# Kernel optimization log

Measured on AMD Instinct MI355X. Metric: run time of the kernel, lower is better.

## Reference

```python
import jax, jax.numpy as jnp
import numpy as np

B, S, D = 2, 1024, 768
H, HD = 12, 64
E, K, F = 8, 2, 3072
EPS = 1e-5


def _ln(x, g, b):
    mu = jnp.mean(x, -1, keepdims=True)
    var = jnp.mean(jnp.square(x - mu), -1, keepdims=True)
    return (x - mu) * jax.lax.rsqrt(var + EPS) * g + b


def setup_inputs() -> dict:
    key = jax.random.key(0)
    ks = jax.random.split(key, 12)
    s = lambda k, shape, sc: jax.random.normal(k, shape, jnp.float32) * sc
    return {
        "hidden_states": s(ks[0], (B, S, D), 1.0),
        "ln1_g": jnp.ones((D,), jnp.float32), "ln1_b": jnp.zeros((D,), jnp.float32),
        "w_attn": s(ks[1], (D, 3 * D), 0.02), "b_attn": jnp.zeros((3 * D,), jnp.float32),
        "w_attnproj": s(ks[2], (D, D), 0.02), "b_attnproj": jnp.zeros((D,), jnp.float32),
        "ln2_g": jnp.ones((D,), jnp.float32), "ln2_b": jnp.zeros((D,), jnp.float32),
        "w_router": s(ks[3], (E, D), 0.01),
        "w_fc": s(ks[4], (E, D, F), 0.02 / E), "b_fc": jnp.zeros((E, F), jnp.float32),
        "w_proj": s(ks[5], (E, F, D), 0.02 / E), "b_proj": jnp.zeros((E, D), jnp.float32),
    }


def reference(hidden_states, ln1_g, ln1_b, w_attn, b_attn, w_attnproj, b_attnproj,
              ln2_g, ln2_b, w_router, w_fc, b_fc, w_proj, b_proj):
    # --- attention sub-block (GPT-2 style, causal) ---
    residual = hidden_states
    x = _ln(hidden_states, ln1_g, ln1_b)
    qkv = x @ w_attn + b_attn                         # [B,S,3D]
    q, k, v = jnp.split(qkv, 3, axis=-1)
    def heads(t):
        return t.reshape(B, S, H, HD).transpose(0, 2, 1, 3)  # [B,H,S,HD]
    q, k, v = heads(q), heads(k), heads(v)
    scores = jnp.einsum("bhqd,bhkd->bhqk", q, k) / np.sqrt(HD).astype(np.float32)
    causal = jnp.tril(jnp.ones((S, S), bool))
    scores = jnp.where(causal, scores, jnp.finfo(scores.dtype).min)
    attn = jax.nn.softmax(scores, axis=-1)
    ctx = jnp.einsum("bhqk,bhkd->bhqd", attn, v)
    ctx = ctx.transpose(0, 2, 1, 3).reshape(B, S, D)
    attn_out = ctx @ w_attnproj + b_attnproj
    hs = attn_out + residual

    # --- MoE FFN sub-block ---
    residual = hs
    x2 = _ln(hs, ln2_g, ln2_b)
    logits = x2 @ w_router.T                          # [B,S,E]
    probs = jax.nn.softmax(logits, axis=-1)
    top_w, top_idx = jax.lax.top_k(probs, K)          # [B,S,K]
    top_w = top_w / jnp.sum(top_w, -1, keepdims=True)
    gates = jnp.sum(jax.nn.one_hot(top_idx, E, dtype=x2.dtype) * top_w[..., None], axis=2)  # [B,S,E]
    h = jax.nn.gelu(jnp.einsum("bsd,edf->bsef", x2, w_fc) + b_fc, approximate=False)
    y = jnp.einsum("bsef,efd->bsed", h, w_proj) + b_proj
    moe_out = jnp.einsum("bse,bsed->bsd", gates, y)
    return moe_out + residual
```

## Files before the change

### kernel.cpp

```cpp
#include <hip/hip_runtime.h>
#include <hip/hip_bf16.h>
#include <math.h>

#define NB 2
#define SEQ 1024
#define DM 768
#define NHEAD 12
#define HDIM 64
#define NEXP 8
#define FF 3072
#define NTOK (NB*SEQ)
#define TDIM (3*DM)
#define LNEPS 1e-5f

typedef __attribute__((ext_vector_type(8))) short v8s;
typedef __attribute__((ext_vector_type(4))) float v4f;

#define GLDS16(src, dst) \
    __builtin_amdgcn_global_load_lds((const __attribute__((address_space(1))) unsigned int*)(src), \
                                     (__attribute__((address_space(3))) unsigned int*)(dst), 16, 0, 0)

static __device__ __forceinline__ float bf2f(unsigned short u){
    return __uint_as_float(((unsigned)u) << 16);
}
static __device__ __forceinline__ unsigned short f2bf(float f){
    unsigned u = __float_as_uint(f);
    u += 0x7fffu + ((u >> 16) & 1u);
    return (unsigned short)(u >> 16);
}
static __device__ __forceinline__ float gelu_exact(float x){
    return 0.5f * x * (1.0f + erff(x * 0.70710678118654752440f));
}

__global__ __launch_bounds__(256) void tconv_kernel(const float* __restrict__ in,
                                                    unsigned short* __restrict__ out,
                                                    int R, int C){
    __shared__ float T[32][33];
    size_t base = (size_t)blockIdx.z * R * C;
    int c0 = blockIdx.x * 32, r0 = blockIdx.y * 32;
    int t = threadIdx.x;
    int tr = t >> 3, tc4 = (t & 7) * 4;
    float4 v = *(const float4*)&in[base + (size_t)(r0 + tr) * C + c0 + tc4];
    T[tr][tc4+0] = v.x; T[tr][tc4+1] = v.y; T[tr][tc4+2] = v.z; T[tr][tc4+3] = v.w;
    __syncthreads();
    int oc = t >> 3, or4 = (t & 7) * 4;
    ushort4 o;
    o.x = f2bf(T[or4+0][oc]); o.y = f2bf(T[or4+1][oc]);
    o.z = f2bf(T[or4+2][oc]); o.w = f2bf(T[or4+3][oc]);
    *(ushort4*)&out[base + (size_t)(c0 + oc) * R + r0 + or4] = o;
}

__global__ __launch_bounds__(256) void ln_kernel(const float* __restrict__ in,
                                                 const float* __restrict__ g,
                                                 const float* __restrict__ b,
                                                 float* __restrict__ out,
                                                 unsigned short* __restrict__ outb){
    int t = blockIdx.x;
    const float* row = in + (size_t)t * DM;
    int tid = threadIdx.x;
    float v0 = row[tid], v1 = row[tid + 256], v2 = row[tid + 512];
    float s  = v0 + v1 + v2;
    float ss = v0*v0 + v1*v1 + v2*v2;
    for (int off = 32; off; off >>= 1){
        s  += __shfl_down(s, off);
        ss += __shfl_down(ss, off);
    }
    __shared__ float ls[4], lss[4];
    int wid = tid >> 6, lane = tid & 63;
    if (lane == 0){ ls[wid] = s; lss[wid] = ss; }
    __syncthreads();
    if (tid == 0){
        float a = ls[0] + ls[1] + ls[2] + ls[3];
        float c = lss[0] + lss[1] + lss[2] + lss[3];
        float mu = a / (float)DM;
        float var = c / (float)DM - mu * mu;
        ls[0] = mu; lss[0] = rsqrtf(var + LNEPS);
    }
    __syncthreads();
    float mu = ls[0], rs = lss[0];
    float* orow = out + (size_t)t * DM;
    unsigned short* obrow = outb + (size_t)t * DM;
    float o0 = (v0 - mu) * rs * g[tid]       + b[tid];
    float o1 = (v1 - mu) * rs * g[tid + 256] + b[tid + 256];
    float o2 = (v2 - mu) * rs * g[tid + 512] + b[tid + 512];
    orow[tid] = o0; orow[tid+256] = o1; orow[tid+512] = o2;
    obrow[tid] = f2bf(o0); obrow[tid+256] = f2bf(o1); obrow[tid+512] = f2bf(o2);
}


__global__ __launch_bounds__(256) void mm_qkv(const unsigned short* __restrict__ Ab,
                                              const unsigned short* __restrict__ Bb,
                                              const float* __restrict__ bias,
                                              float* __restrict__ C){
    __shared__ __align__(16) unsigned short As[128*32];
    __shared__ __align__(16) unsigned short Bs[128*32];
    int bm = blockIdx.y * 128, bn = blockIdx.x * 128;
    int tid = threadIdx.x, wave = tid >> 6, lane = tid & 63;
    int quad = lane >> 4, l15 = lane & 15;
    int wm = wave >> 1, wn = wave & 1;
    int lrow = lane >> 2, lchunk = (lane & 3) * 8;
    const unsigned short* aS0 = Ab + (size_t)(bm +      wave*16 + lrow) * 768 + lchunk;
    const unsigned short* aS1 = Ab + (size_t)(bm + 64 + wave*16 + lrow) * 768 + lchunk;
    const unsigned short* bS0 = Bb + (size_t)(bn +      wave*16 + lrow) * 768 + lchunk;
    const unsigned short* bS1 = Bb + (size_t)(bn + 64 + wave*16 + lrow) * 768 + lchunk;
    unsigned short* aD0 = &As[(     wave*16)*32];
    unsigned short* aD1 = &As[(64 + wave*16)*32];
    unsigned short* bD0 = &Bs[(     wave*16)*32];
    unsigned short* bD1 = &Bs[(64 + wave*16)*32];
    v4f acc[4][4];
    #pragma unroll
    for (int i = 0; i < 4; i++)
        #pragma unroll
        for (int j = 0; j < 4; j++) acc[i][j] = (v4f){0.f,0.f,0.f,0.f};
    for (int kt = 0; kt < 768/32; kt++){
        int kb = kt * 32;
        GLDS16(aS0 + kb, aD0); GLDS16(aS1 + kb, aD1);
        GLDS16(bS0 + kb, bD0); GLDS16(bS1 + kb, bD1);
        __syncthreads();
        v8s a[4], b[4];
        #pragma unroll
        for (int i = 0; i < 4; i++){
            a[i] = *(const v8s*)&As[(wm*64 + i*16 + l15)*32 + quad*8];
            b[i] = *(const v8s*)&Bs[(wn*64 + i*16 + l15)*32 + quad*8];
        }
        #pragma unroll
        for (int mt = 0; mt < 4; mt++)
            #pragma unroll
            for (int nt = 0; nt < 4; nt++)
                acc[mt][nt] = __builtin_amdgcn_mfma_f32_16x16x32_bf16(a[mt], b[nt], acc[mt][nt], 0, 0, 0);
        __syncthreads();
    }
    #pragma unroll
    for (int nt = 0; nt < 4; nt++){
        int n = bn + wn*64 + nt*16 + l15;
        float bb = bias[n];
        #pragma unroll
        for (int mt = 0; mt < 4; mt++){
            int m = bm + wm*64 + mt*16 + quad*4;
            #pragma unroll
            for (int r = 0; r < 4; r++)
                C[(size_t)(m + r) * TDIM + n] = acc[mt][nt][r] + bb;
        }
    }
}

__global__ __launch_bounds__(256) void mm_attnproj(const unsigned short* __restrict__ Ab,
                                                   const unsigned short* __restrict__ Bb,
                                                   const float* __restrict__ bias,
                                                   const float* __restrict__ res,
                                                   float* __restrict__ C){
    __shared__ __align__(16) unsigned short As[128*32];
    __shared__ __align__(16) unsigned short Bs[128*32];
    int bm = blockIdx.y * 128, bn = blockIdx.x * 128;
    int tid = threadIdx.x, wave = tid >> 6, lane = tid & 63;
    int quad = lane >> 4, l15 = lane & 15;
    int wm = wave >> 1, wn = wave & 1;
    int lrow = lane >> 2, lchunk = (lane & 3) * 8;
    const unsigned short* aS0 = Ab + (size_t)(bm +      wave*16 + lrow) * 768 + lchunk;
    const unsigned short* aS1 = Ab + (size_t)(bm + 64 + wave*16 + lrow) * 768 + lchunk;
    const unsigned short* bS0 = Bb + (size_t)(bn +      wave*16 + lrow) * 768 + lchunk;
    const unsigned short* bS1 = Bb + (size_t)(bn + 64 + wave*16 + lrow) * 768 + lchunk;
    unsigned short* aD0 = &As[(     wave*16)*32];
    unsigned short* aD1 = &As[(64 + wave*16)*32];
    unsigned short* bD0 = &Bs[(     wave*16)*32];
    unsigned short* bD1 = &Bs[(64 + wave*16)*32];
    v4f acc[4][4];
    #pragma unroll
    for (int i = 0; i < 4; i++)
        #pragma unroll
        for (int j = 0; j < 4; j++) acc[i][j] = (v4f){0.f,0.f,0.f,0.f};
    for (int kt = 0; kt < 768/32; kt++){
        int kb = kt * 32;
        GLDS16(aS0 + kb, aD0); GLDS16(aS1 + kb, aD1);
        GLDS16(bS0 + kb, bD0); GLDS16(bS1 + kb, bD1);
        __syncthreads();
        v8s a[4], b[4];
        #pragma unroll
        for (int i = 0; i < 4; i++){
            a[i] = *(const v8s*)&As[(wm*64 + i*16 + l15)*32 + quad*8];
            b[i] = *(const v8s*)&Bs[(wn*64 + i*16 + l15)*32 + quad*8];
        }
        #pragma unroll
        for (int mt = 0; mt < 4; mt++)
            #pragma unroll
            for (int nt = 0; nt < 4; nt++)
                acc[mt][nt] = __builtin_amdgcn_mfma_f32_16x16x32_bf16(a[mt], b[nt], acc[mt][nt], 0, 0, 0);
        __syncthreads();
    }
    #pragma unroll
    for (int nt = 0; nt < 4; nt++){
        int n = bn + wn*64 + nt*16 + l15;
        float bb = bias[n];
        #pragma unroll
        for (int mt = 0; mt < 4; mt++){
            int m = bm + wm*64 + mt*16 + quad*4;
            #pragma unroll
            for (int r = 0; r < 4; r++)
                C[(size_t)(m + r) * DM + n] = acc[mt][nt][r] + bb + res[(size_t)(m + r) * DM + n];
        }
    }
}

__global__ __launch_bounds__(256) void mm_fc(const unsigned short* __restrict__ Xb,
                                             const unsigned short* __restrict__ Wb,
                                             const float* __restrict__ bfc,
                                             const int* __restrict__ expTok,
                                             const int* __restrict__ cnt,
                                             const int* __restrict__ offE,
                                             unsigned short* __restrict__ H){
    int e = blockIdx.z, tile = blockIdx.y;
    int c = cnt[e];
    int rows = c - tile * 128;
    if (rows <= 0) return;
    __shared__ __align__(16) unsigned short As[128*32];
    __shared__ __align__(16) unsigned short Bs[128*32];
    __shared__ int toks[128];
    int bn = blockIdx.x * 128;
    int tid = threadIdx.x, wave = tid >> 6, lane = tid & 63;
    if (tid < 128){
        int idx = tile * 128 + tid;
        if (idx >= c) idx = c - 1;
        toks[tid] = expTok[e * NTOK + idx];
    }
    __syncthreads();
    int quad = lane >> 4, l15 = lane & 15;
    int wm = wave >> 1, wn = wave & 1;
    int lrow = lane >> 2, lchunk = (lane & 3) * 8;
    int tok0 = toks[     wave*16 + lrow];
    int tok1 = toks[64 + wave*16 + lrow];
    const unsigned short* Be = Wb + (size_t)e * FF * DM;
    const unsigned short* aS0 = Xb + (size_t)tok0 * 768 + lchunk;
    const unsigned short* aS1 = Xb + (size_t)tok1 * 768 + lchunk;
    const unsigned short* bS0 = Be + (size_t)(bn +      wave*16 + lrow) * 768 + lchunk;
    const unsigned short* bS1 = Be + (size_t)(bn + 64 + wave*16 + lrow) * 768 + lchunk;
    unsigned short* aD0 = &As[(     wave*16)*32];
    unsigned short* aD1 = &As[(64 + wave*16)*32];
    unsigned short* bD0 = &Bs[(     wave*16)*32];
    unsigned short* bD1 = &Bs[(64 + wave*16)*32];
    v4f acc[4][4];
    #pragma unroll
    for (int i = 0; i < 4; i++)
        #pragma unroll
        for (int j = 0; j < 4; j++) acc[i][j] = (v4f){0.f,0.f,0.f,0.f};
    for (int kt = 0; kt < 768/32; kt++){
        int kb = kt * 32;
        GLDS16(aS0 + kb, aD0); GLDS16(aS1 + kb, aD1);
        GLDS16(bS0 + kb, bD0); GLDS16(bS1 + kb, bD1);
        __syncthreads();
        v8s a[4], b[4];
        #pragma unroll
        for (int i = 0; i < 4; i++){
            a[i] = *(const v8s*)&As[(wm*64 + i*16 + l15)*32 + quad*8];
            b[i] = *(const v8s*)&Bs[(wn*64 + i*16 + l15)*32 + quad*8];
        }
        #pragma unroll
        for (int mt = 0; mt < 4; mt++)
            #pragma unroll
            for (int nt = 0; nt < 4; nt++)
                acc[mt][nt] = __builtin_amdgcn_mfma_f32_16x16x32_bf16(a[mt], b[nt], acc[mt][nt], 0, 0, 0);
        __syncthreads();
    }
    int slot0 = offE[e] + tile * 128;
    #pragma unroll
    for (int nt = 0; nt < 4; nt++){
        int n = bn + wn*64 + nt*16 + l15;
        float bb = bfc[(size_t)e * FF + n];
        #pragma unroll
        for (int mt = 0; mt < 4; mt++){
            int ml = wm*64 + mt*16 + quad*4;
            #pragma unroll
            for (int r = 0; r < 4; r++)
                if (ml + r < rows)
                    H[(size_t)(slot0 + ml + r) * FF + n] = f2bf(gelu_exact(acc[mt][nt][r] + bb));
        }
    }
}

__global__ __launch_bounds__(256) void mm_proj(const unsigned short* __restrict__ H,
                                               const unsigned short* __restrict__ Wb,
                                               const int* __restrict__ cnt,
                                               const int* __restrict__ offE,
                                               float* __restrict__ Y){
    int e = blockIdx.z, tile = blockIdx.y;
    int c = cnt[e];
    int rows = c - tile * 128;
    if (rows <= 0) return;
    __shared__ __align__(16) unsigned short As[128*32];
    __shared__ __align__(16) unsigned short Bs[128*32];
    int bn = blockIdx.x * 128;
    int tid = threadIdx.x, wave = tid >> 6, lane = tid & 63;
    int quad = lane >> 4, l15 = lane & 15;
    int wm = wave >> 1, wn = wave & 1;
    int lrow = lane >> 2, lchunk = (lane & 3) * 8;
    int slot0 = offE[e] + tile * 128;
    int rl0 =      wave*16 + lrow; if (rl0 > rows - 1) rl0 = rows - 1;
    int rl1 = 64 + wave*16 + lrow; if (rl1 > rows - 1) rl1 = rows - 1;
    const unsigned short* Be = Wb + (size_t)e * DM * FF;
    const unsigned short* aS0 = H + (size_t)(slot0 + rl0) * FF + lchunk;
    const unsigned short* aS1 = H + (size_t)(slot0 + rl1) * FF + lchunk;
    const unsigned short* bS0 = Be + (size_t)(bn +      wave*16 + lrow) * FF + lchunk;
    const unsigned short* bS1 = Be + (size_t)(bn + 64 + wave*16 + lrow) * FF + lchunk;
    unsigned short* aD0 = &As[(     wave*16)*32];
    unsigned short* aD1 = &As[(64 + wave*16)*32];
    unsigned short* bD0 = &Bs[(     wave*16)*32];
    unsigned short* bD1 = &Bs[(64 + wave*16)*32];
    v4f acc[4][4];
    #pragma unroll
    for (int i = 0; i < 4; i++)
        #pragma unroll
        for (int j = 0; j < 4; j++) acc[i][j] = (v4f){0.f,0.f,0.f,0.f};
    for (int kt = 0; kt < FF/32; kt++){
        int kb = kt * 32;
        GLDS16(aS0 + kb, aD0); GLDS16(aS1 + kb, aD1);
        GLDS16(bS0 + kb, bD0); GLDS16(bS1 + kb, bD1);
        __syncthreads();
        v8s a[4], b[4];
        #pragma unroll
        for (int i = 0; i < 4; i++){
            a[i] = *(const v8s*)&As[(wm*64 + i*16 + l15)*32 + quad*8];
            b[i] = *(const v8s*)&Bs[(wn*64 + i*16 + l15)*32 + quad*8];
        }
        #pragma unroll
        for (int mt = 0; mt < 4; mt++)
            #pragma unroll
            for (int nt = 0; nt < 4; nt++)
                acc[mt][nt] = __builtin_amdgcn_mfma_f32_16x16x32_bf16(a[mt], b[nt], acc[mt][nt], 0, 0, 0);
        __syncthreads();
    }
    #pragma unroll
    for (int nt = 0; nt < 4; nt++){
        int n = bn + wn*64 + nt*16 + l15;
        #pragma unroll
        for (int mt = 0; mt < 4; mt++){
            int ml = wm*64 + mt*16 + quad*4;
            #pragma unroll
            for (int r = 0; r < 4; r++)
                if (ml + r < rows)
                    Y[(size_t)(slot0 + ml + r) * DM + n] = acc[mt][nt][r];
        }
    }
}

__global__ __launch_bounds__(256) void attn_prep(const float* __restrict__ qkv,
                                                 unsigned short* __restrict__ Qb,
                                                 unsigned short* __restrict__ Kb,
                                                 unsigned short* __restrict__ Vt){
    int bi = blockIdx.x;
    int c = bi & 15, bh = bi >> 4;
    int h = bh % NHEAD, b = bh / NHEAD;
    __shared__ float vt[64][65];
    int tid = threadIdx.x;
    int row = tid >> 2, ds = (tid & 3) * 16;
    const float* base = qkv + (size_t)(b*SEQ + c*64 + row) * TDIM + h*HDIM + ds;
    size_t qkrow = ((size_t)bh*SEQ + c*64 + row) * HDIM + ds;
    #pragma unroll
    for (int j = 0; j < 16; j += 4){
        float4 qv = *(const float4*)(base + j);
        ushort4 qo;
        qo.x = f2bf(qv.x*0.125f); qo.y = f2bf(qv.y*0.125f);
        qo.z = f2bf(qv.z*0.125f); qo.w = f2bf(qv.w*0.125f);
        *(ushort4*)&Qb[qkrow + j] = qo;
        float4 kv = *(const float4*)(base + DM + j);
        ushort4 ko;
        ko.x = f2bf(kv.x); ko.y = f2bf(kv.y); ko.z = f2bf(kv.z); ko.w = f2bf(kv.w);
        *(ushort4*)&Kb[qkrow + j] = ko;
        float4 vv = *(const float4*)(base + 2*DM + j);
        vt[row][ds+j+0] = vv.x; vt[row][ds+j+1] = vv.y;
        vt[row][ds+j+2] = vv.z; vt[row][ds+j+3] = vv.w;
    }
    __syncthreads();
    int d = tid >> 2, ks = (tid & 3) * 16;
    size_t vrow = ((size_t)bh*HDIM + d) * SEQ + c*64 + ks;
    #pragma unroll
    for (int j = 0; j < 16; j += 4){
        ushort4 o;
        o.x = f2bf(vt[ks+j+0][d]); o.y = f2bf(vt[ks+j+1][d]);
        o.z = f2bf(vt[ks+j+2][d]); o.w = f2bf(vt[ks+j+3][d]);
        *(ushort4*)&Vt[vrow + j] = o;
    }
}

__global__ __launch_bounds__(64) void fattn(const unsigned short* __restrict__ Qb,
                                            const unsigned short* __restrict__ Kb,
                                            const unsigned short* __restrict__ Vt,
                                            unsigned short* __restrict__ ctxb){
    int bh = blockIdx.x >> 6;
    int q0 = (63 - (blockIdx.x & 63)) * 16;
    int h = bh % NHEAD, b = bh / NHEAD;
    int lane = threadIdx.x;
    int quad = lane >> 4, l15 = lane & 15;

    __shared__ __align__(16) unsigned short Plds[16*32];

    const unsigned short* qp = Qb + ((size_t)bh*SEQ + q0 + l15) * HDIM + quad*8;
    v8s qa0 = *(const v8s*)qp;
    v8s qa1 = *(const v8s*)(qp + 32);

    v4f o0 = {0,0,0,0}, o1 = {0,0,0,0}, o2 = {0,0,0,0}, o3 = {0,0,0,0};
    float mrow[4] = {-1e30f,-1e30f,-1e30f,-1e30f};
    float lrow[4] = {0,0,0,0};

    int nch = (q0 + 16 + 31) >> 5;
    for (int ch = 0; ch < nch; ch++){
        int kt = ch * 32;
        const unsigned short* kp = Kb + ((size_t)bh*SEQ + kt + l15) * HDIM + quad*8;
        v8s kb0l = *(const v8s*)kp;
        v8s kb0h = *(const v8s*)(kp + 32);
        v8s kb1l = *(const v8s*)(kp + 16*HDIM);
        v8s kb1h = *(const v8s*)(kp + 16*HDIM + 32);
        v4f s0 = {0,0,0,0}, s1 = {0,0,0,0};
        s0 = __builtin_amdgcn_mfma_f32_16x16x32_bf16(qa0, kb0l, s0, 0, 0, 0);
        s0 = __builtin_amdgcn_mfma_f32_16x16x32_bf16(qa1, kb0h, s0, 0, 0, 0);
        s1 = __builtin_amdgcn_mfma_f32_16x16x32_bf16(qa0, kb1l, s1, 0, 0, 0);
        s1 = __builtin_amdgcn_mfma_f32_16x16x32_bf16(qa1, kb1h, s1, 0, 0, 0);

        int key0 = kt + l15, key1 = kt + 16 + l15;
        float alpha[4];
        #pragma unroll
        for (int r = 0; r < 4; r++){
            int qrow = q0 + quad*4 + r;
            float v0 = (key0 <= qrow) ? s0[r] : -1e30f;
            float v1 = (key1 <= qrow) ? s1[r] : -1e30f;
            float mx = fmaxf(v0, v1);
            mx = fmaxf(mx, __shfl_xor(mx, 1));
            mx = fmaxf(mx, __shfl_xor(mx, 2));
            mx = fmaxf(mx, __shfl_xor(mx, 4));
            mx = fmaxf(mx, __shfl_xor(mx, 8));
            float mn = fmaxf(mrow[r], mx);
            alpha[r] = __expf(mrow[r] - mn);
            float p0 = __expf(v0 - mn);
            float p1 = __expf(v1 - mn);
            float ps = p0 + p1;
            ps += __shfl_xor(ps, 1);
            ps += __shfl_xor(ps, 2);
            ps += __shfl_xor(ps, 4);
            ps += __shfl_xor(ps, 8);
            lrow[r] = lrow[r] * alpha[r] + ps;
            mrow[r] = mn;
            Plds[(quad*4 + r)*32 + l15]      = f2bf(p0);
            Plds[(quad*4 + r)*32 + 16 + l15] = f2bf(p1);
        }
        #pragma unroll
        for (int r = 0; r < 4; r++){
            o0[r] *= alpha[r]; o1[r] *= alpha[r];
            o2[r] *= alpha[r]; o3[r] *= alpha[r];
        }
        __syncthreads();
        v8s pa = *(const v8s*)&Plds[l15*32 + quad*8];
        const unsigned short* vp = Vt + ((size_t)bh*HDIM + l15) * SEQ + kt + quad*8;
        v8s vb0 = *(const v8s*)vp;
        v8s vb1 = *(const v8s*)(vp + 16*SEQ);
        v8s vb2 = *(const v8s*)(vp + 32*SEQ);
        v8s vb3 = *(const v8s*)(vp + 48*SEQ);
        o0 = __builtin_amdgcn_mfma_f32_16x16x32_bf16(pa, vb0, o0, 0, 0, 0);
        o1 = __builtin_amdgcn_mfma_f32_16x16x32_bf16(pa, vb1, o1, 0, 0, 0);
        o2 = __builtin_amdgcn_mfma_f32_16x16x32_bf16(pa, vb2, o2, 0, 0, 0);
        o3 = __builtin_amdgcn_mfma_f32_16x16x32_bf16(pa, vb3, o3, 0, 0, 0);
        __syncthreads();
    }
    #pragma unroll
    for (int r = 0; r < 4; r++){
        float inv = 1.0f / lrow[r];
        size_t orow = (size_t)(b*SEQ + q0 + quad*4 + r) * DM + h*HDIM;
        ctxb[orow + l15]      = f2bf(o0[r] * inv);
        ctxb[orow + 16 + l15] = f2bf(o1[r] * inv);
        ctxb[orow + 32 + l15] = f2bf(o2[r] * inv);
        ctxb[orow + 48 + l15] = f2bf(o3[r] * inv);
    }
}

__global__ __launch_bounds__(64) void router_kernel(const float* __restrict__ x2,
                                                    const float* __restrict__ wr,
                                                    int* __restrict__ cnt,
                                                    int* __restrict__ expTok,
                                                    int* __restrict__ tokE,
                                                    int* __restrict__ tokPos,
                                                    float* __restrict__ tokGate){
    int t = blockIdx.x;
    int lane = threadIdx.x;
    const float* xr = x2 + (size_t)t * DM;
    float acc[NEXP] = {};
    for (int d = lane; d < DM; d += 64){
        float xv = xr[d];
        #pragma unroll
        for (int e = 0; e < NEXP; e++) acc[e] += xv * wr[e*DM + d];
    }
    #pragma unroll
    for (int e = 0; e < NEXP; e++)
        for (int off = 32; off; off >>= 1) acc[e] += __shfl_xor(acc[e], off);
    if (lane == 0){
        int i0 = 0; float m0 = acc[0];
        #pragma unroll
        for (int e = 1; e < NEXP; e++) if (acc[e] > m0){ m0 = acc[e]; i0 = e; }
        int i1 = -1; float m1 = -INFINITY;
        #pragma unroll
        for (int e = 0; e < NEXP; e++) if (e != i0 && acc[e] > m1){ m1 = acc[e]; i1 = e; }
        float mx = fmaxf(m0, m1);
        float e0 = __expf(m0 - mx), e1 = __expf(m1 - mx);
        float inv = 1.0f / (e0 + e1);
        int p0 = atomicAdd(&cnt[i0], 1);
        int p1 = atomicAdd(&cnt[i1], 1);
        expTok[i0*NTOK + p0] = t;
        expTok[i1*NTOK + p1] = t;
        tokE[t*2]   = i0; tokE[t*2+1]   = i1;
        tokPos[t*2] = p0; tokPos[t*2+1] = p1;
        tokGate[t*2]   = e0 * inv;
        tokGate[t*2+1] = e1 * inv;
    }
}

__global__ void offsets_kernel(const int* __restrict__ cnt, int* __restrict__ offE){
    if (threadIdx.x == 0 && blockIdx.x == 0){
        int a = 0;
        for (int e = 0; e < NEXP; e++){ offE[e] = a; a += cnt[e]; }
    }
}

__global__ __launch_bounds__(256) void combine_kernel(const float* __restrict__ hs,
                                                      const float* __restrict__ Y,
                                                      const float* __restrict__ bproj,
                                                      const int* __restrict__ tokE,
                                                      const int* __restrict__ tokPos,
                                                      const float* __restrict__ tokGate,
                                                      const int* __restrict__ offE,
                                                      float* __restrict__ out){
    int t = blockIdx.x;
    int e0 = tokE[t*2], e1 = tokE[t*2+1];
    int s0 = offE[e0] + tokPos[t*2];
    int s1 = offE[e1] + tokPos[t*2+1];
    float g0 = tokGate[t*2], g1 = tokGate[t*2+1];
    const float* y0 = Y + (size_t)s0 * DM;
    const float* y1 = Y + (size_t)s1 * DM;
    const float* b0 = bproj + (size_t)e0 * DM;
    const float* b1 = bproj + (size_t)e1 * DM;
    const float* hr = hs + (size_t)t * DM;
    float* orow = out + (size_t)t * DM;
    for (int d = threadIdx.x; d < DM; d += 256){
        orow[d] = hr[d] + g0 * (y0[d] + b0[d]) + g1 * (y1[d] + b1[d]);
    }
}

extern "C" void kernel_launch(void* const* d_in, const int* in_sizes, int n_in,
                              void* d_out, int out_size, void* d_ws, size_t ws_size,
                              hipStream_t stream){
    (void)in_sizes; (void)n_in; (void)out_size; (void)ws_size;
    const float* hidden  = (const float*)d_in[0];
    const float* ln1_g   = (const float*)d_in[1];
    const float* ln1_b   = (const float*)d_in[2];
    const float* w_attn  = (const float*)d_in[3];
    const float* b_attn  = (const float*)d_in[4];
    const float* w_aproj = (const float*)d_in[5];
    const float* b_aproj = (const float*)d_in[6];
    const float* ln2_g   = (const float*)d_in[7];
    const float* ln2_b   = (const float*)d_in[8];
    const float* w_rout  = (const float*)d_in[9];
    const float* w_fc    = (const float*)d_in[10];
    const float* b_fc    = (const float*)d_in[11];
    const float* w_proj  = (const float*)d_in[12];
    const float* b_proj  = (const float*)d_in[13];
    float* out = (float*)d_out;

    char* ws = (char*)d_ws;
    float*          x    = (float*)(ws + 0);
    unsigned short* Vt   = (unsigned short*)(ws + 6291456);
    unsigned short* ctxb = (unsigned short*)(ws + 9437184);
    float*          Y    = (float*)(ws + 0);
    float*          hs   = (float*)(ws + 12582912);
    unsigned short* xb   = (unsigned short*)(ws + 18874368);
    float*          qkv  = (float*)(ws + 22020096);
    unsigned short* Qb   = (unsigned short*)(ws + 40894464);
    unsigned short* Kb   = (unsigned short*)(ws + 44040192);
    unsigned short* H    = (unsigned short*)(ws + 22020096);
    unsigned short* Wab  = (unsigned short*)(ws + 47185920);
    unsigned short* Wapb = (unsigned short*)(ws + 50724864);
    unsigned short* Wfcb = (unsigned short*)(ws + 51904512);
    unsigned short* Wprb = (unsigned short*)(ws + 89653248);
    char* rt = ws + 127401984;
    int* cnt      = (int*)(rt + 0);
    int* offE     = (int*)(rt + 64);
    int* expTok   = (int*)(rt + 128);
    int* tokE     = (int*)(rt + 128 + 65536);
    int* tokPos   = (int*)(rt + 128 + 81920);
    float* tokGate= (float*)(rt + 128 + 98304);

    hipMemsetAsync(cnt, 0, NEXP * sizeof(int), stream);

    tconv_kernel<<<dim3(TDIM/32, DM/32, 1), 256, 0, stream>>>(w_attn, Wab, DM, TDIM);
    tconv_kernel<<<dim3(DM/32, DM/32, 1), 256, 0, stream>>>(w_aproj, Wapb, DM, DM);
    tconv_kernel<<<dim3(FF/32, DM/32, NEXP), 256, 0, stream>>>(w_fc, Wfcb, DM, FF);
    tconv_kernel<<<dim3(DM/32, FF/32, NEXP), 256, 0, stream>>>(w_proj, Wprb, FF, DM);

    ln_kernel<<<NTOK, 256, 0, stream>>>(hidden, ln1_g, ln1_b, x, xb);
    mm_qkv<<<dim3(TDIM/128, NTOK/128), 256, 0, stream>>>(xb, Wab, b_attn, qkv);
    attn_prep<<<NB*NHEAD*16, 256, 0, stream>>>(qkv, Qb, Kb, Vt);
    fattn<<<NB*NHEAD*64, 64, 0, stream>>>(Qb, Kb, Vt, ctxb);
    mm_attnproj<<<dim3(DM/128, NTOK/128), 256, 0, stream>>>(ctxb, Wapb, b_aproj, hidden, hs);
    ln_kernel<<<NTOK, 256, 0, stream>>>(hs, ln2_g, ln2_b, x, xb);
    router_kernel<<<NTOK, 64, 0, stream>>>(x, w_rout, cnt, expTok, tokE, tokPos, tokGate);
    offsets_kernel<<<1, 64, 0, stream>>>(cnt, offE);
    mm_fc<<<dim3(FF/128, NTOK/128, NEXP), 256, 0, stream>>>(xb, Wfcb, b_fc, expTok, cnt, offE, H);
    mm_proj<<<dim3(DM/128, NTOK/128, NEXP), 256, 0, stream>>>(H, Wprb, cnt, offE, Y);
    combine_kernel<<<NTOK, 256, 0, stream>>>(hs, Y, b_proj, tokE, tokPos, tokGate, offE, out);
}
```

Baseline: 520.2 us.

## Fuse QKV epilogue into head layout, fuse LN with router, retile GEMMs, split-K proj

The QKV GEMM now writes bf16 Q (prescaled), K and transposed V directly, which removes the fp32 qkv buffer and the attn_prep kernel. The second layernorm is fused with the router, so the fp32 normalized activations are no longer written out. Flash attention now processes 32 query rows per wave and attnproj/qkv use smaller tiles for more blocks. The expert down-projection is split along K into two partial outputs that the combine kernel sums. Together these cut launches and intermediate memory traffic, at the cost of extra partial-sum reads and more complex indexing.

```diff
diff --git a/kernel.cpp b/kernel.cpp
--- a/kernel.cpp
+++ b/kernel.cpp
@@ -12,6 +12,7 @@
 #define NTOK (NB*SEQ)
 #define TDIM (3*DM)
 #define LNEPS 1e-5f
+#define NSLOT (NTOK*2)
 
 typedef __attribute__((ext_vector_type(8))) short v8s;
 typedef __attribute__((ext_vector_type(4))) float v4f;
@@ -50,11 +51,10 @@
     *(ushort4*)&out[base + (size_t)(c0 + oc) * R + r0 + or4] = o;
 }
 
-__global__ __launch_bounds__(256) void ln_kernel(const float* __restrict__ in,
-                                                 const float* __restrict__ g,
-                                                 const float* __restrict__ b,
-                                                 float* __restrict__ out,
-                                                 unsigned short* __restrict__ outb){
+__global__ __launch_bounds__(256) void ln_b(const float* __restrict__ in,
+                                            const float* __restrict__ g,
+                                            const float* __restrict__ b,
+                                            unsigned short* __restrict__ outb){
     int t = blockIdx.x;
     const float* row = in + (size_t)t * DM;
     int tid = threadIdx.x;
@@ -78,68 +78,264 @@
     }
     __syncthreads();
     float mu = ls[0], rs = lss[0];
-    float* orow = out + (size_t)t * DM;
     unsigned short* obrow = outb + (size_t)t * DM;
+    obrow[tid]     = f2bf((v0 - mu) * rs * g[tid]       + b[tid]);
+    obrow[tid+256] = f2bf((v1 - mu) * rs * g[tid + 256] + b[tid + 256]);
+    obrow[tid+512] = f2bf((v2 - mu) * rs * g[tid + 512] + b[tid + 512]);
+}
+
+__global__ __launch_bounds__(256) void ln_router(const float* __restrict__ in,
+                                                 const float* __restrict__ g,
+                                                 const float* __restrict__ b,
+                                                 const float* __restrict__ wr,
+                                                 unsigned short* __restrict__ outb,
+                                                 int* __restrict__ cnt,
+                                                 int* __restrict__ expTok,
+                                                 int* __restrict__ tokE,
+                                                 int* __restrict__ tokPos,
+                                                 float* __restrict__ tokGate){
+    int t = blockIdx.x;
+    const float* row = in + (size_t)t * DM;
+    int tid = threadIdx.x;
+    float v0 = row[tid], v1 = row[tid + 256], v2 = row[tid + 512];
+    float s  = v0 + v1 + v2;
+    float ss = v0*v0 + v1*v1 + v2*v2;
+    for (int off = 32; off; off >>= 1){
+        s  += __shfl_down(s, off);
+        ss += __shfl_down(ss, off);
+    }
+    __shared__ float ls[4], lss[4];
+    __shared__ float wsum[4][NEXP];
+    int wid = tid >> 6, lane = tid & 63;
+    if (lane == 0){ ls[wid] = s; lss[wid] = ss; }
+    __syncthreads();
+    if (tid == 0){
+        float a = ls[0] + ls[1] + ls[2] + ls[3];
+        float c = lss[0] + lss[1] + lss[2] + lss[3];
+        float mu = a / (float)DM;
+        float var = c / (float)DM - mu * mu;
+        ls[0] = mu; lss[0] = rsqrtf(var + LNEPS);
+    }
+    __syncthreads();
+    float mu = ls[0], rs = lss[0];
     float o0 = (v0 - mu) * rs * g[tid]       + b[tid];
     float o1 = (v1 - mu) * rs * g[tid + 256] + b[tid + 256];
     float o2 = (v2 - mu) * rs * g[tid + 512] + b[tid + 512];
-    orow[tid] = o0; orow[tid+256] = o1; orow[tid+512] = o2;
+    unsigned short* obrow = outb + (size_t)t * DM;
     obrow[tid] = f2bf(o0); obrow[tid+256] = f2bf(o1); obrow[tid+512] = f2bf(o2);
-}
-
+    float p[NEXP];
+    #pragma unroll
+    for (int e = 0; e < NEXP; e++)
+        p[e] = o0*wr[e*DM + tid] + o1*wr[e*DM + tid + 256] + o2*wr[e*DM + tid + 512];
+    #pragma unroll
+    for (int e = 0; e < NEXP; e++)
+        for (int off = 32; off; off >>= 1) p[e] += __shfl_down(p[e], off);
+    if (lane == 0){
+        #pragma unroll
+        for (int e = 0; e < NEXP; e++) wsum[wid][e] = p[e];
+    }
+    __syncthreads();
+    if (tid == 0){
+        float lg[NEXP];
+        #pragma unroll
+        for (int e = 0; e < NEXP; e++)
+            lg[e] = wsum[0][e] + wsum[1][e] + wsum[2][e] + wsum[3][e];
+        int i0 = 0; float m0 = lg[0];
+        #pragma unroll
+        for (int e = 1; e < NEXP; e++) if (lg[e] > m0){ m0 = lg[e]; i0 = e; }
+        int i1 = -1; float m1 = -INFINITY;
+        #pragma unroll
+        for (int e = 0; e < NEXP; e++) if (e != i0 && lg[e] > m1){ m1 = lg[e]; i1 = e; }
+        float mx = fmaxf(m0, m1);
+        float e0 = __expf(m0 - mx), e1 = __expf(m1 - mx);
+        float inv = 1.0f / (e0 + e1);
+        int p0 = atomicAdd(&cnt[i0], 1);
+        int p1 = atomicAdd(&cnt[i1], 1);
+        expTok[i0*NTOK + p0] = t;
+        expTok[i1*NTOK + p1] = t;
+        tokE[t*2]   = i0; tokE[t*2+1]   = i1;
+        tokPos[t*2] = p0; tokPos[t*2+1] = p1;
+        tokGate[t*2]   = e0 * inv;
+        tokGate[t*2+1] = e1 * inv;
+    }
+}
 
 __global__ __launch_bounds__(256) void mm_qkv(const unsigned short* __restrict__ Ab,
                                               const unsigned short* __restrict__ Bb,
                                               const float* __restrict__ bias,
-                                              float* __restrict__ C){
-    __shared__ __align__(16) unsigned short As[128*32];
+                                              unsigned short* __restrict__ Qb,
+                                              unsigned short* __restrict__ Kb,
+                                              unsigned short* __restrict__ Vt){
+    __shared__ __align__(16) unsigned short As[64*32];
     __shared__ __align__(16) unsigned short Bs[128*32];
-    int bm = blockIdx.y * 128, bn = blockIdx.x * 128;
+    int bm = blockIdx.y * 64, bn = blockIdx.x * 128;
     int tid = threadIdx.x, wave = tid >> 6, lane = tid & 63;
     int quad = lane >> 4, l15 = lane & 15;
     int wm = wave >> 1, wn = wave & 1;
+    int arow = tid >> 2, achunk = (tid & 3) * 8;
     int lrow = lane >> 2, lchunk = (lane & 3) * 8;
-    const unsigned short* aS0 = Ab + (size_t)(bm +      wave*16 + lrow) * 768 + lchunk;
-    const unsigned short* aS1 = Ab + (size_t)(bm + 64 + wave*16 + lrow) * 768 + lchunk;
-    const unsigned short* bS0 = Bb + (size_t)(bn +      wave*16 + lrow) * 768 + lchunk;
-    const unsigned short* bS1 = Bb + (size_t)(bn + 64 + wave*16 + lrow) * 768 + lchunk;
-    unsigned short* aD0 = &As[(     wave*16)*32];
-    unsigned short* aD1 = &As[(64 + wave*16)*32];
+    const unsigned short* aS  = Ab + (size_t)(bm + arow) * DM + achunk;
+    const unsigned short* bS0 = Bb + (size_t)(bn +      wave*16 + lrow) * DM + lchunk;
+    const unsigned short* bS1 = Bb + (size_t)(bn + 64 + wave*16 + lrow) * DM + lchunk;
+    unsigned short* aD  = &As[(wave*16)*32];
     unsigned short* bD0 = &Bs[(     wave*16)*32];
     unsigned short* bD1 = &Bs[(64 + wave*16)*32];
-    v4f acc[4][4];
-    #pragma unroll
-    for (int i = 0; i < 4; i++)
+    v4f acc[2][4];
+    #pragma unroll
+    for (int i = 0; i < 2; i++)
         #pragma unroll
         for (int j = 0; j < 4; j++) acc[i][j] = (v4f){0.f,0.f,0.f,0.f};
-    for (int kt = 0; kt < 768/32; kt++){
+    for (int kt = 0; kt < DM/32; kt++){
         int kb = kt * 32;
-        GLDS16(aS0 + kb, aD0); GLDS16(aS1 + kb, aD1);
-        GLDS16(bS0 + kb, bD0); GLDS16(bS1 + kb, bD1);
-        __syncthreads();
-        v8s a[4], b[4];
-        #pragma unroll
-        for (int i = 0; i < 4; i++){
-            a[i] = *(const v8s*)&As[(wm*64 + i*16 + l15)*32 + quad*8];
-            b[i] = *(const v8s*)&Bs[(wn*64 + i*16 + l15)*32 + quad*8];
-        }
-        #pragma unroll
-        for (int mt = 0; mt < 4; mt++)
-            #pragma unroll
-            for (int nt = 0; nt < 4; nt++)
-                acc[mt][nt] = __builtin_amdgcn_mfma_f32_16x16x32_bf16(a[mt], b[nt], acc[mt][nt], 0, 0, 0);
-        __syncthreads();
-    }
-    #pragma unroll
-    for (int nt = 0; nt < 4; nt++){
-        int n = bn + wn*64 + nt*16 + l15;
+        GLDS16(aS + kb, aD); GLDS16(bS0 + kb, bD0); GLDS16(bS1 + kb, bD1);
+        __syncthreads();
+        v8s a[2], bfr[4];
+        #pragma unroll
+        for (int i = 0; i < 2; i++) a[i] = *(const v8s*)&As[(wm*32 + i*16 + l15)*32 + quad*8];
+        #pragma unroll
+        for (int i = 0; i < 4; i++) bfr[i] = *(const v8s*)&Bs[(wn*64 + i*16 + l15)*32 + quad*8];
+        #pragma unroll
+        for (int mi = 0; mi < 2; mi++)
+            #pragma unroll
+            for (int ni = 0; ni < 4; ni++)
+                acc[mi][ni] = __builtin_amdgcn_mfma_f32_16x16x32_bf16(a[mi], bfr[ni], acc[mi][ni], 0, 0, 0);
+        __syncthreads();
+    }
+    int btyp = bn / DM;
+    #pragma unroll
+    for (int ni = 0; ni < 4; ni++){
+        int n = bn + wn*64 + ni*16 + l15;
         float bb = bias[n];
-        #pragma unroll
-        for (int mt = 0; mt < 4; mt++){
-            int m = bm + wm*64 + mt*16 + quad*4;
-            #pragma unroll
-            for (int r = 0; r < 4; r++)
-                C[(size_t)(m + r) * TDIM + n] = acc[mt][nt][r] + bb;
+        int hd = n % DM; int h = hd >> 6; int d = hd & 63;
+        #pragma unroll
+        for (int mi = 0; mi < 2; mi++){
+            int m = bm + wm*32 + mi*16 + quad*4;
+            int b = m >> 10, sd = m & 1023;
+            size_t bhbase = (size_t)(b*NHEAD + h);
+            if (btyp == 0){
+                #pragma unroll
+                for (int r = 0; r < 4; r++)
+                    Qb[(bhbase*SEQ + sd + r)*HDIM + d] = f2bf((acc[mi][ni][r] + bb) * 0.125f);
+            } else if (btyp == 1){
+                #pragma unroll
+                for (int r = 0; r < 4; r++)
+                    Kb[(bhbase*SEQ + sd + r)*HDIM + d] = f2bf(acc[mi][ni][r] + bb);
+            } else {
+                ushort4 o;
+                o.x = f2bf(acc[mi][ni][0] + bb); o.y = f2bf(acc[mi][ni][1] + bb);
+                o.z = f2bf(acc[mi][ni][2] + bb); o.w = f2bf(acc[mi][ni][3] + bb);
+                *(ushort4*)&Vt[(bhbase*HDIM + d)*SEQ + sd] = o;
+            }
+        }
+    }
+}
+
+__global__ __launch_bounds__(64) void fattn(const unsigned short* __restrict__ Qb,
+                                            const unsigned short* __restrict__ Kb,
+                                            const unsigned short* __restrict__ Vt,
+                                            unsigned short* __restrict__ ctxb){
+    int bh = blockIdx.x >> 5;
+    int q0 = (31 - (blockIdx.x & 31)) * 32;
+    int h = bh % NHEAD, b = bh / NHEAD;
+    int lane = threadIdx.x;
+    int quad = lane >> 4, l15 = lane & 15;
+
+    __shared__ __align__(16) unsigned short Plds[32*32];
+
+    const unsigned short* qp = Qb + ((size_t)bh*SEQ + q0 + l15) * HDIM + quad*8;
+    v8s qa00 = *(const v8s*)qp;
+    v8s qa01 = *(const v8s*)(qp + 32);
+    v8s qa10 = *(const v8s*)(qp + 16*HDIM);
+    v8s qa11 = *(const v8s*)(qp + 16*HDIM + 32);
+
+    v4f o[2][4];
+    #pragma unroll
+    for (int i = 0; i < 2; i++)
+        #pragma unroll
+        for (int j = 0; j < 4; j++) o[i][j] = (v4f){0.f,0.f,0.f,0.f};
+    float mrow[2][4], lrow[2][4];
+    #pragma unroll
+    for (int i = 0; i < 2; i++)
+        #pragma unroll
+        for (int r = 0; r < 4; r++){ mrow[i][r] = -1e30f; lrow[i][r] = 0.f; }
+
+    int nch = (q0 >> 5) + 1;
+    for (int ch = 0; ch < nch; ch++){
+        int kt = ch * 32;
+        const unsigned short* kp = Kb + ((size_t)bh*SEQ + kt + l15) * HDIM + quad*8;
+        v8s k00 = *(const v8s*)kp;
+        v8s k01 = *(const v8s*)(kp + 32);
+        v8s k10 = *(const v8s*)(kp + 16*HDIM);
+        v8s k11 = *(const v8s*)(kp + 16*HDIM + 32);
+        v4f s00 = {0,0,0,0}, s01 = {0,0,0,0}, s10 = {0,0,0,0}, s11 = {0,0,0,0};
+        s00 = __builtin_amdgcn_mfma_f32_16x16x32_bf16(qa00, k00, s00, 0, 0, 0);
+        s00 = __builtin_amdgcn_mfma_f32_16x16x32_bf16(qa01, k01, s00, 0, 0, 0);
+        s01 = __builtin_amdgcn_mfma_f32_16x16x32_bf16(qa00, k10, s01, 0, 0, 0);
+        s01 = __builtin_amdgcn_mfma_f32_16x16x32_bf16(qa01, k11, s01, 0, 0, 0);
+        s10 = __builtin_amdgcn_mfma_f32_16x16x32_bf16(qa10, k00, s10, 0, 0, 0);
+        s10 = __builtin_amdgcn_mfma_f32_16x16x32_bf16(qa11, k01, s10, 0, 0, 0);
+        s11 = __builtin_amdgcn_mfma_f32_16x16x32_bf16(qa10, k10, s11, 0, 0, 0);
+        s11 = __builtin_amdgcn_mfma_f32_16x16x32_bf16(qa11, k11, s11, 0, 0, 0);
+
+        int key0 = kt + l15, key1 = kt + 16 + l15;
+        float alpha[2][4];
+        #pragma unroll
+        for (int mi = 0; mi < 2; mi++){
+            #pragma unroll
+            for (int r = 0; r < 4; r++){
+                int qrow = q0 + mi*16 + quad*4 + r;
+                float sv0 = mi ? s10[r] : s00[r];
+                float sv1 = mi ? s11[r] : s01[r];
+                float v0 = (key0 <= qrow) ? sv0 : -1e30f;
+                float v1 = (key1 <= qrow) ? sv1 : -1e30f;
+                float mx = fmaxf(v0, v1);
+                mx = fmaxf(mx, __shfl_xor(mx, 1));
+                mx = fmaxf(mx, __shfl_xor(mx, 2));
+                mx = fmaxf(mx, __shfl_xor(mx, 4));
+                mx = fmaxf(mx, __shfl_xor(mx, 8));
+                float mn = fmaxf(mrow[mi][r], mx);
+                alpha[mi][r] = __expf(mrow[mi][r] - mn);
+                float p0 = __expf(v0 - mn);
+                float p1 = __expf(v1 - mn);
+                float ps = p0 + p1;
+                ps += __shfl_xor(ps, 1);
+                ps += __shfl_xor(ps, 2);
+                ps += __shfl_xor(ps, 4);
+                ps += __shfl_xor(ps, 8);
+                lrow[mi][r] = lrow[mi][r] * alpha[mi][r] + ps;
+                mrow[mi][r] = mn;
+                Plds[(mi*16 + quad*4 + r)*32 + l15]      = f2bf(p0);
+                Plds[(mi*16 + quad*4 + r)*32 + 16 + l15] = f2bf(p1);
+            }
+        }
+        #pragma unroll
+        for (int mi = 0; mi < 2; mi++)
+            #pragma unroll
+            for (int df = 0; df < 4; df++)
+                #pragma unroll
+                for (int r = 0; r < 4; r++)
+                    o[mi][df][r] *= alpha[mi][r];
+        __syncthreads();
+        v8s pa0 = *(const v8s*)&Plds[l15*32 + quad*8];
+        v8s pa1 = *(const v8s*)&Plds[(16 + l15)*32 + quad*8];
+        const unsigned short* vp = Vt + ((size_t)bh*HDIM + l15) * SEQ + kt + quad*8;
+        #pragma unroll
+        for (int df = 0; df < 4; df++){
+            v8s vb = *(const v8s*)(vp + df*16*SEQ);
+            o[0][df] = __builtin_amdgcn_mfma_f32_16x16x32_bf16(pa0, vb, o[0][df], 0, 0, 0);
+            o[1][df] = __builtin_amdgcn_mfma_f32_16x16x32_bf16(pa1, vb, o[1][df], 0, 0, 0);
+        }
+        __syncthreads();
+    }
+    #pragma unroll
+    for (int mi = 0; mi < 2; mi++){
+        #pragma unroll
+        for (int r = 0; r < 4; r++){
+            float inv = 1.0f / lrow[mi][r];
+            size_t orow = (size_t)(b*SEQ + q0 + mi*16 + quad*4 + r) * DM + h*HDIM;
+            #pragma unroll
+            for (int df = 0; df < 4; df++)
+                ctxb[orow + df*16 + l15] = f2bf(o[mi][df][r] * inv);
         }
     }
 }
@@ -149,54 +345,49 @@
                                                    const float* __restrict__ bias,
                                                    const float* __restrict__ res,
                                                    float* __restrict__ C){
-    __shared__ __align__(16) unsigned short As[128*32];
-    __shared__ __align__(16) unsigned short Bs[128*32];
-    int bm = blockIdx.y * 128, bn = blockIdx.x * 128;
+    __shared__ __align__(16) unsigned short As[64*32];
+    __shared__ __align__(16) unsigned short Bs[64*32];
+    int bm = blockIdx.y * 64, bn = blockIdx.x * 64;
     int tid = threadIdx.x, wave = tid >> 6, lane = tid & 63;
     int quad = lane >> 4, l15 = lane & 15;
     int wm = wave >> 1, wn = wave & 1;
-    int lrow = lane >> 2, lchunk = (lane & 3) * 8;
-    const unsigned short* aS0 = Ab + (size_t)(bm +      wave*16 + lrow) * 768 + lchunk;
-    const unsigned short* aS1 = Ab + (size_t)(bm + 64 + wave*16 + lrow) * 768 + lchunk;
-    const unsigned short* bS0 = Bb + (size_t)(bn +      wave*16 + lrow) * 768 + lchunk;
-    const unsigned short* bS1 = Bb + (size_t)(bn + 64 + wave*16 + lrow) * 768 + lchunk;
-    unsigned short* aD0 = &As[(     wave*16)*32];
-    unsigned short* aD1 = &As[(64 + wave*16)*32];
-    unsigned short* bD0 = &Bs[(     wave*16)*32];
-    unsigned short* bD1 = &Bs[(64 + wave*16)*32];
-    v4f acc[4][4];
-    #pragma unroll
-    for (int i = 0; i < 4; i++)
-        #pragma unroll
-        for (int j = 0; j < 4; j++) acc[i][j] = (v4f){0.f,0.f,0.f,0.f};
-    for (int kt = 0; kt < 768/32; kt++){
+    int arow = tid >> 2, achunk = (tid & 3) * 8;
+    const unsigned short* aS = Ab + (size_t)(bm + arow) * DM + achunk;
+    const unsigned short* bS = Bb + (size_t)(bn + arow) * DM + achunk;
+    unsigned short* aD = &As[(wave*16)*32];
+    unsigned short* bD = &Bs[(wave*16)*32];
+    v4f acc[2][2];
+    #pragma unroll
+    for (int i = 0; i < 2; i++)
+        #pragma unroll
+        for (int j = 0; j < 2; j++) acc[i][j] = (v4f){0.f,0.f,0.f,0.f};
+    for (int kt = 0; kt < DM/32; kt++){
         int kb = kt * 32;
-        GLDS16(aS0 + kb, aD0); GLDS16(aS1 + kb, aD1);
-        GLDS16(bS0 + kb, bD0); GLDS16(bS1 + kb, bD1);
-        __syncthreads();
-        v8s a[4], b[4];
-        #pragma unroll
-        for (int i = 0; i < 4; i++){
-            a[i] = *(const v8s*)&As[(wm*64 + i*16 + l15)*32 + quad*8];
-            b[i] = *(const v8s*)&Bs[(wn*64 + i*16 + l15)*32 + quad*8];
-        }
-        #pragma unroll
-        for (int mt = 0; mt < 4; mt++)
-            #pragma unroll
-            for (int nt = 0; nt < 4; nt++)
-                acc[mt][nt] = __builtin_amdgcn_mfma_f32_16x16x32_bf16(a[mt], b[nt], acc[mt][nt], 0, 0, 0);
-        __syncthreads();
-    }
-    #pragma unroll
-    for (int nt = 0; nt < 4; nt++){
-        int n = bn + wn*64 + nt*16 + l15;
+        GLDS16(aS + kb, aD); GLDS16(bS + kb, bD);
+        __syncthreads();
+        v8s a[2], bfr[2];
+        #pragma unroll
+        for (int i = 0; i < 2; i++){
+            a[i]   = *(const v8s*)&As[(wm*32 + i*16 + l15)*32 + quad*8];
+            bfr[i] = *(const v8s*)&Bs[(wn*32 + i*16 + l15)*32 + quad*8];
+        }
+        #pragma unroll
+        for (int mi = 0; mi < 2; mi++)
+            #pragma unroll
+            for (int ni = 0; ni < 2; ni++)
+                acc[mi][ni] = __builtin_amdgcn_mfma_f32_16x16x32_bf16(a[mi], bfr[ni], acc[mi][ni], 0, 0, 0);
+        __syncthreads();
+    }
+    #pragma unroll
+    for (int ni = 0; ni < 2; ni++){
+        int n = bn + wn*32 + ni*16 + l15;
         float bb = bias[n];
         #pragma unroll
-        for (int mt = 0; mt < 4; mt++){
-            int m = bm + wm*64 + mt*16 + quad*4;
+        for (int mi = 0; mi < 2; mi++){
+            int m = bm + wm*32 + mi*16 + quad*4;
             #pragma unroll
             for (int r = 0; r < 4; r++)
-                C[(size_t)(m + r) * DM + n] = acc[mt][nt][r] + bb + res[(size_t)(m + r) * DM + n];
+                C[(size_t)(m + r) * DM + n] = acc[mi][ni][r] + bb + res[(size_t)(m + r) * DM + n];
         }
     }
 }
@@ -229,10 +420,10 @@
     int tok0 = toks[     wave*16 + lrow];
     int tok1 = toks[64 + wave*16 + lrow];
     const unsigned short* Be = Wb + (size_t)e * FF * DM;
-    const unsigned short* aS0 = Xb + (size_t)tok0 * 768 + lchunk;
-    const unsigned short* aS1 = Xb + (size_t)tok1 * 768 + lchunk;
-    const unsigned short* bS0 = Be + (size_t)(bn +      wave*16 + lrow) * 768 + lchunk;
-    const unsigned short* bS1 = Be + (size_t)(bn + 64 + wave*16 + lrow) * 768 + lchunk;
+    const unsigned short* aS0 = Xb + (size_t)tok0 * DM + lchunk;
+    const unsigned short* aS1 = Xb + (size_t)tok1 * DM + lchunk;
+    const unsigned short* bS0 = Be + (size_t)(bn +      wave*16 + lrow) * DM + lchunk;
+    const unsigned short* bS1 = Be + (size_t)(bn + 64 + wave*16 + lrow) * DM + lchunk;
     unsigned short* aD0 = &As[(     wave*16)*32];
     unsigned short* aD1 = &As[(64 + wave*16)*32];
     unsigned short* bD0 = &Bs[(     wave*16)*32];
@@ -242,22 +433,22 @@
     for (int i = 0; i < 4; i++)
         #pragma unroll
         for (int j = 0; j < 4; j++) acc[i][j] = (v4f){0.f,0.f,0.f,0.f};
-    for (int kt = 0; kt < 768/32; kt++){
+    for (int kt = 0; kt < DM/32; kt++){
         int kb = kt * 32;
         GLDS16(aS0 + kb, aD0); GLDS16(aS1 + kb, aD1);
         GLDS16(bS0 + kb, bD0); GLDS16(bS1 + kb, bD1);
         __syncthreads();
-        v8s a[4], b[4];
+        v8s a[4], bfr[4];
         #pragma unroll
         for (int i = 0; i < 4; i++){
-            a[i] = *(const v8s*)&As[(wm*64 + i*16 + l15)*32 + quad*8];
-            b[i] = *(const v8s*)&Bs[(wn*64 + i*16 + l15)*32 + quad*8];
+            a[i]   = *(const v8s*)&As[(wm*64 + i*16 + l15)*32 + quad*8];
+            bfr[i] = *(const v8s*)&Bs[(wn*64 + i*16 + l15)*32 + quad*8];
         }
         #pragma unroll
         for (int mt = 0; mt < 4; mt++)
             #pragma unroll
             for (int nt = 0; nt < 4; nt++)
-                acc[mt][nt] = __builtin_amdgcn_mfma_f32_16x16x32_bf16(a[mt], b[nt], acc[mt][nt], 0, 0, 0);
+                acc[mt][nt] = __builtin_amdgcn_mfma_f32_16x16x32_bf16(a[mt], bfr[nt], acc[mt][nt], 0, 0, 0);
         __syncthreads();
     }
     int slot0 = offE[e] + tile * 128;
@@ -280,232 +471,62 @@
                                                const unsigned short* __restrict__ Wb,
                                                const int* __restrict__ cnt,
                                                const int* __restrict__ offE,
-                                               float* __restrict__ Y){
+                                               float* __restrict__ Yp){
     int e = blockIdx.z, tile = blockIdx.y;
     int c = cnt[e];
-    int rows = c - tile * 128;
+    int rows = c - tile * 64;
     if (rows <= 0) return;
-    __shared__ __align__(16) unsigned short As[128*32];
+    int sk = blockIdx.x & 1;
+    int bn = (blockIdx.x >> 1) * 128;
+    __shared__ __align__(16) unsigned short As[64*32];
     __shared__ __align__(16) unsigned short Bs[128*32];
-    int bn = blockIdx.x * 128;
     int tid = threadIdx.x, wave = tid >> 6, lane = tid & 63;
     int quad = lane >> 4, l15 = lane & 15;
     int wm = wave >> 1, wn = wave & 1;
+    int slot0 = offE[e] + tile * 64;
+    int arow = tid >> 2, achunk = (tid & 3) * 8;
+    int arl = arow < rows ? arow : rows - 1;
     int lrow = lane >> 2, lchunk = (lane & 3) * 8;
-    int slot0 = offE[e] + tile * 128;
-    int rl0 =      wave*16 + lrow; if (rl0 > rows - 1) rl0 = rows - 1;
-    int rl1 = 64 + wave*16 + lrow; if (rl1 > rows - 1) rl1 = rows - 1;
     const unsigned short* Be = Wb + (size_t)e * DM * FF;
-    const unsigned short* aS0 = H + (size_t)(slot0 + rl0) * FF + lchunk;
-    const unsigned short* aS1 = H + (size_t)(slot0 + rl1) * FF + lchunk;
-    const unsigned short* bS0 = Be + (size_t)(bn +      wave*16 + lrow) * FF + lchunk;
-    const unsigned short* bS1 = Be + (size_t)(bn + 64 + wave*16 + lrow) * FF + lchunk;
-    unsigned short* aD0 = &As[(     wave*16)*32];
-    unsigned short* aD1 = &As[(64 + wave*16)*32];
+    const unsigned short* aS  = H  + (size_t)(slot0 + arl) * FF + sk*1536 + achunk;
+    const unsigned short* bS0 = Be + (size_t)(bn +      wave*16 + lrow) * FF + sk*1536 + lchunk;
+    const unsigned short* bS1 = Be + (size_t)(bn + 64 + wave*16 + lrow) * FF + sk*1536 + lchunk;
+    unsigned short* aD  = &As[(wave*16)*32];
     unsigned short* bD0 = &Bs[(     wave*16)*32];
     unsigned short* bD1 = &Bs[(64 + wave*16)*32];
-    v4f acc[4][4];
-    #pragma unroll
-    for (int i = 0; i < 4; i++)
+    v4f acc[2][4];
+    #pragma unroll
+    for (int i = 0; i < 2; i++)
         #pragma unroll
         for (int j = 0; j < 4; j++) acc[i][j] = (v4f){0.f,0.f,0.f,0.f};
-    for (int kt = 0; kt < FF/32; kt++){
+    for (int kt = 0; kt < 1536/32; kt++){
         int kb = kt * 32;
-        GLDS16(aS0 + kb, aD0); GLDS16(aS1 + kb, aD1);
-        GLDS16(bS0 + kb, bD0); GLDS16(bS1 + kb, bD1);
-        __syncthreads();
-        v8s a[4], b[4];
-        #pragma unroll
-        for (int i = 0; i < 4; i++){
-            a[i] = *(const v8s*)&As[(wm*64 + i*16 + l15)*32 + quad*8];
-            b[i] = *(const v8s*)&Bs[(wn*64 + i*16 + l15)*32 + quad*8];
-        }
-        #pragma unroll
-        for (int mt = 0; mt < 4; mt++)
-            #pragma unroll
-            for (int nt = 0; nt < 4; nt++)
-                acc[mt][nt] = __builtin_amdgcn_mfma_f32_16x16x32_bf16(a[mt], b[nt], acc[mt][nt], 0, 0, 0);
-        __syncthreads();
-    }
-    #pragma unroll
-    for (int nt = 0; nt < 4; nt++){
-        int n = bn + wn*64 + nt*16 + l15;
-        #pragma unroll
-        for (int mt = 0; mt < 4; mt++){
-            int ml = wm*64 + mt*16 + quad*4;
+        GLDS16(aS + kb, aD); GLDS16(bS0 + kb, bD0); GLDS16(bS1 + kb, bD1);
+        __syncthreads();
+        v8s a[2], bfr[4];
+        #pragma unroll
+        for (int i = 0; i < 2; i++) a[i] = *(const v8s*)&As[(wm*32 + i*16 + l15)*32 + quad*8];
+        #pragma unroll
+        for (int i = 0; i < 4; i++) bfr[i] = *(const v8s*)&Bs[(wn*64 + i*16 + l15)*32 + quad*8];
+        #pragma unroll
+        for (int mi = 0; mi < 2; mi++)
+            #pragma unroll
+            for (int ni = 0; ni < 4; ni++)
+                acc[mi][ni] = __builtin_amdgcn_mfma_f32_16x16x32_bf16(a[mi], bfr[ni], acc[mi][ni], 0, 0, 0);
+        __syncthreads();
+    }
+    float* Yo = Yp + (size_t)sk * NSLOT * DM;
+    #pragma unroll
+    for (int ni = 0; ni < 4; ni++){
+        int n = bn + wn*64 + ni*16 + l15;
+        #pragma unroll
+        for (int mi = 0; mi < 2; mi++){
+            int ml = wm*32 + mi*16 + quad*4;
             #pragma unroll
             for (int r = 0; r < 4; r++)
                 if (ml + r < rows)
-                    Y[(size_t)(slot0 + ml + r) * DM + n] = acc[mt][nt][r];
-        }
-    }
-}
-
-__global__ __launch_bounds__(256) void attn_prep(const float* __restrict__ qkv,
-                                                 unsigned short* __restrict__ Qb,
-                                                 unsigned short* __restrict__ Kb,
-                                                 unsigned short* __restrict__ Vt){
-    int bi = blockIdx.x;
-    int c = bi & 15, bh = bi >> 4;
-    int h = bh % NHEAD, b = bh / NHEAD;
-    __shared__ float vt[64][65];
-    int tid = threadIdx.x;
-    int row = tid >> 2, ds = (tid & 3) * 16;
-    const float* base = qkv + (size_t)(b*SEQ + c*64 + row) * TDIM + h*HDIM + ds;
-    size_t qkrow = ((size_t)bh*SEQ + c*64 + row) * HDIM + ds;
-    #pragma unroll
-    for (int j = 0; j < 16; j += 4){
-        float4 qv = *(const float4*)(base + j);
-        ushort4 qo;
-        qo.x = f2bf(qv.x*0.125f); qo.y = f2bf(qv.y*0.125f);
-        qo.z = f2bf(qv.z*0.125f); qo.w = f2bf(qv.w*0.125f);
-        *(ushort4*)&Qb[qkrow + j] = qo;
-        float4 kv = *(const float4*)(base + DM + j);
-        ushort4 ko;
-        ko.x = f2bf(kv.x); ko.y = f2bf(kv.y); ko.z = f2bf(kv.z); ko.w = f2bf(kv.w);
-        *(ushort4*)&Kb[qkrow + j] = ko;
-        float4 vv = *(const float4*)(base + 2*DM + j);
-        vt[row][ds+j+0] = vv.x; vt[row][ds+j+1] = vv.y;
-        vt[row][ds+j+2] = vv.z; vt[row][ds+j+3] = vv.w;
-    }
-    __syncthreads();
-    int d = tid >> 2, ks = (tid & 3) * 16;
-    size_t vrow = ((size_t)bh*HDIM + d) * SEQ + c*64 + ks;
-    #pragma unroll
-    for (int j = 0; j < 16; j += 4){
-        ushort4 o;
-        o.x = f2bf(vt[ks+j+0][d]); o.y = f2bf(vt[ks+j+1][d]);
-        o.z = f2bf(vt[ks+j+2][d]); o.w = f2bf(vt[ks+j+3][d]);
-        *(ushort4*)&Vt[vrow + j] = o;
-    }
-}
-
-__global__ __launch_bounds__(64) void fattn(const unsigned short* __restrict__ Qb,
-                                            const unsigned short* __restrict__ Kb,
-                                            const unsigned short* __restrict__ Vt,
-                                            unsigned short* __restrict__ ctxb){
-    int bh = blockIdx.x >> 6;
-    int q0 = (63 - (blockIdx.x & 63)) * 16;
-    int h = bh % NHEAD, b = bh / NHEAD;
-    int lane = threadIdx.x;
-    int quad = lane >> 4, l15 = lane & 15;
-
-    __shared__ __align__(16) unsigned short Plds[16*32];
-
-    const unsigned short* qp = Qb + ((size_t)bh*SEQ + q0 + l15) * HDIM + quad*8;
-    v8s qa0 = *(const v8s*)qp;
-    v8s qa1 = *(const v8s*)(qp + 32);
-
-    v4f o0 = {0,0,0,0}, o1 = {0,0,0,0}, o2 = {0,0,0,0}, o3 = {0,0,0,0};
-    float mrow[4] = {-1e30f,-1e30f,-1e30f,-1e30f};
-    float lrow[4] = {0,0,0,0};
-
-    int nch = (q0 + 16 + 31) >> 5;
-    for (int ch = 0; ch < nch; ch++){
-        int kt = ch * 32;
-        const unsigned short* kp = Kb + ((size_t)bh*SEQ + kt + l15) * HDIM + quad*8;
-        v8s kb0l = *(const v8s*)kp;
-        v8s kb0h = *(const v8s*)(kp + 32);
-        v8s kb1l = *(const v8s*)(kp + 16*HDIM);
-        v8s kb1h = *(const v8s*)(kp + 16*HDIM + 32);
-        v4f s0 = {0,0,0,0}, s1 = {0,0,0,0};
-        s0 = __builtin_amdgcn_mfma_f32_16x16x32_bf16(qa0, kb0l, s0, 0, 0, 0);
-        s0 = __builtin_amdgcn_mfma_f32_16x16x32_bf16(qa1, kb0h, s0, 0, 0, 0);
-        s1 = __builtin_amdgcn_mfma_f32_16x16x32_bf16(qa0, kb1l, s1, 0, 0, 0);
-        s1 = __builtin_amdgcn_mfma_f32_16x16x32_bf16(qa1, kb1h, s1, 0, 0, 0);
-
-        int key0 = kt + l15, key1 = kt + 16 + l15;
-        float alpha[4];
-        #pragma unroll
-        for (int r = 0; r < 4; r++){
-            int qrow = q0 + quad*4 + r;
-            float v0 = (key0 <= qrow) ? s0[r] : -1e30f;
-            float v1 = (key1 <= qrow) ? s1[r] : -1e30f;
-            float mx = fmaxf(v0, v1);
-            mx = fmaxf(mx, __shfl_xor(mx, 1));
-            mx = fmaxf(mx, __shfl_xor(mx, 2));
-            mx = fmaxf(mx, __shfl_xor(mx, 4));
-            mx = fmaxf(mx, __shfl_xor(mx, 8));
-            float mn = fmaxf(mrow[r], mx);
-            alpha[r] = __expf(mrow[r] - mn);
-            float p0 = __expf(v0 - mn);
-            float p1 = __expf(v1 - mn);
-            float ps = p0 + p1;
-            ps += __shfl_xor(ps, 1);
-            ps += __shfl_xor(ps, 2);
-            ps += __shfl_xor(ps, 4);
-            ps += __shfl_xor(ps, 8);
-            lrow[r] = lrow[r] * alpha[r] + ps;
-            mrow[r] = mn;
-            Plds[(quad*4 + r)*32 + l15]      = f2bf(p0);
-            Plds[(quad*4 + r)*32 + 16 + l15] = f2bf(p1);
-        }
-        #pragma unroll
-        for (int r = 0; r < 4; r++){
-            o0[r] *= alpha[r]; o1[r] *= alpha[r];
-            o2[r] *= alpha[r]; o3[r] *= alpha[r];
-        }
-        __syncthreads();
-        v8s pa = *(const v8s*)&Plds[l15*32 + quad*8];
-        const unsigned short* vp = Vt + ((size_t)bh*HDIM + l15) * SEQ + kt + quad*8;
-        v8s vb0 = *(const v8s*)vp;
-        v8s vb1 = *(const v8s*)(vp + 16*SEQ);
-        v8s vb2 = *(const v8s*)(vp + 32*SEQ);
-        v8s vb3 = *(const v8s*)(vp + 48*SEQ);
-        o0 = __builtin_amdgcn_mfma_f32_16x16x32_bf16(pa, vb0, o0, 0, 0, 0);
-        o1 = __builtin_amdgcn_mfma_f32_16x16x32_bf16(pa, vb1, o1, 0, 0, 0);
-        o2 = __builtin_amdgcn_mfma_f32_16x16x32_bf16(pa, vb2, o2, 0, 0, 0);
-        o3 = __builtin_amdgcn_mfma_f32_16x16x32_bf16(pa, vb3, o3, 0, 0, 0);
-        __syncthreads();
-    }
-    #pragma unroll
-    for (int r = 0; r < 4; r++){
-        float inv = 1.0f / lrow[r];
-        size_t orow = (size_t)(b*SEQ + q0 + quad*4 + r) * DM + h*HDIM;
-        ctxb[orow + l15]      = f2bf(o0[r] * inv);
-        ctxb[orow + 16 + l15] = f2bf(o1[r] * inv);
-        ctxb[orow + 32 + l15] = f2bf(o2[r] * inv);
-        ctxb[orow + 48 + l15] = f2bf(o3[r] * inv);
-    }
-}
-
-__global__ __launch_bounds__(64) void router_kernel(const float* __restrict__ x2,
-                                                    const float* __restrict__ wr,
-                                                    int* __restrict__ cnt,
-                                                    int* __restrict__ expTok,
-                                                    int* __restrict__ tokE,
-                                                    int* __restrict__ tokPos,
-                                                    float* __restrict__ tokGate){
-    int t = blockIdx.x;
-    int lane = threadIdx.x;
-    const float* xr = x2 + (size_t)t * DM;
-    float acc[NEXP] = {};
-    for (int d = lane; d < DM; d += 64){
-        float xv = xr[d];
-        #pragma unroll
-        for (int e = 0; e < NEXP; e++) acc[e] += xv * wr[e*DM + d];
-    }
-    #pragma unroll
-    for (int e = 0; e < NEXP; e++)
-        for (int off = 32; off; off >>= 1) acc[e] += __shfl_xor(acc[e], off);
-    if (lane == 0){
-        int i0 = 0; float m0 = acc[0];
-        #pragma unroll
-        for (int e = 1; e < NEXP; e++) if (acc[e] > m0){ m0 = acc[e]; i0 = e; }
-        int i1 = -1; float m1 = -INFINITY;
-        #pragma unroll
-        for (int e = 0; e < NEXP; e++) if (e != i0 && acc[e] > m1){ m1 = acc[e]; i1 = e; }
-        float mx = fmaxf(m0, m1);
-        float e0 = __expf(m0 - mx), e1 = __expf(m1 - mx);
-        float inv = 1.0f / (e0 + e1);
-        int p0 = atomicAdd(&cnt[i0], 1);
-        int p1 = atomicAdd(&cnt[i1], 1);
-        expTok[i0*NTOK + p0] = t;
-        expTok[i1*NTOK + p1] = t;
-        tokE[t*2]   = i0; tokE[t*2+1]   = i1;
-        tokPos[t*2] = p0; tokPos[t*2+1] = p1;
-        tokGate[t*2]   = e0 * inv;
-        tokGate[t*2+1] = e1 * inv;
+                    Yo[(size_t)(slot0 + ml + r) * DM + n] = acc[mi][ni][r];
+        }
     }
 }
 
@@ -517,7 +538,7 @@
 }
 
 __global__ __launch_bounds__(256) void combine_kernel(const float* __restrict__ hs,
-                                                      const float* __restrict__ Y,
+                                                      const float* __restrict__ Yp,
                                                       const float* __restrict__ bproj,
                                                       const int* __restrict__ tokE,
                                                       const int* __restrict__ tokPos,
@@ -529,14 +550,16 @@
     int s0 = offE[e0] + tokPos[t*2];
     int s1 = offE[e1] + tokPos[t*2+1];
     float g0 = tokGate[t*2], g1 = tokGate[t*2+1];
-    const float* y0 = Y + (size_t)s0 * DM;
-    const float* y1 = Y + (size_t)s1 * DM;
+    const float* y0a = Yp + (size_t)s0 * DM;
+    const float* y0b = Yp + (size_t)NSLOT * DM + (size_t)s0 * DM;
+    const float* y1a = Yp + (size_t)s1 * DM;
+    const float* y1b = Yp + (size_t)NSLOT * DM + (size_t)s1 * DM;
     const float* b0 = bproj + (size_t)e0 * DM;
     const float* b1 = bproj + (size_t)e1 * DM;
     const float* hr = hs + (size_t)t * DM;
     float* orow = out + (size_t)t * DM;
     for (int d = threadIdx.x; d < DM; d += 256){
-        orow[d] = hr[d] + g0 * (y0[d] + b0[d]) + g1 * (y1[d] + b1[d]);
+        orow[d] = hr[d] + g0 * (y0a[d] + y0b[d] + b0[d]) + g1 * (y1a[d] + y1b[d] + b1[d]);
     }
 }
 
@@ -561,21 +584,19 @@
     float* out = (float*)d_out;
 
     char* ws = (char*)d_ws;
-    float*          x    = (float*)(ws + 0);
-    unsigned short* Vt   = (unsigned short*)(ws + 6291456);
-    unsigned short* ctxb = (unsigned short*)(ws + 9437184);
-    float*          Y    = (float*)(ws + 0);
-    float*          hs   = (float*)(ws + 12582912);
-    unsigned short* xb   = (unsigned short*)(ws + 18874368);
-    float*          qkv  = (float*)(ws + 22020096);
-    unsigned short* Qb   = (unsigned short*)(ws + 40894464);
-    unsigned short* Kb   = (unsigned short*)(ws + 44040192);
-    unsigned short* H    = (unsigned short*)(ws + 22020096);
-    unsigned short* Wab  = (unsigned short*)(ws + 47185920);
-    unsigned short* Wapb = (unsigned short*)(ws + 50724864);
-    unsigned short* Wfcb = (unsigned short*)(ws + 51904512);
-    unsigned short* Wprb = (unsigned short*)(ws + 89653248);
-    char* rt = ws + 127401984;
+    float*          hs   = (float*)(ws + 0);
+    unsigned short* xb   = (unsigned short*)(ws + 6291456);
+    unsigned short* Qb   = (unsigned short*)(ws + 9437184);
+    unsigned short* Kb   = (unsigned short*)(ws + 12582912);
+    unsigned short* Vt   = (unsigned short*)(ws + 15728640);
+    unsigned short* ctxb = (unsigned short*)(ws + 18874368);
+    unsigned short* Wab  = (unsigned short*)(ws + 22020096);
+    unsigned short* Wapb = (unsigned short*)(ws + 25559040);
+    unsigned short* H    = (unsigned short*)(ws + 9437184);
+    unsigned short* Wfcb = (unsigned short*)(ws + 34603008);
+    unsigned short* Wprb = (unsigned short*)(ws + 72351744);
+    float*          Yp   = (float*)(ws + 34603008);
+    char* rt = ws + 110100480;
     int* cnt      = (int*)(rt + 0);
     int* offE     = (int*)(rt + 64);
     int* expTok   = (int*)(rt + 128);
@@ -590,15 +611,14 @@
     tconv_kernel<<<dim3(FF/32, DM/32, NEXP), 256, 0, stream>>>(w_fc, Wfcb, DM, FF);
     tconv_kernel<<<dim3(DM/32, FF/32, NEXP), 256, 0, stream>>>(w_proj, Wprb, FF, DM);
 
-    ln_kernel<<<NTOK, 256, 0, stream>>>(hidden, ln1_g, ln1_b, x, xb);
-    mm_qkv<<<dim3(TDIM/128, NTOK/128), 256, 0, stream>>>(xb, Wab, b_attn, qkv);
-    attn_prep<<<NB*NHEAD*16, 256, 0, stream>>>(qkv, Qb, Kb, Vt);
-    fattn<<<NB*NHEAD*64, 64, 0, stream>>>(Qb, Kb, Vt, ctxb);
-    mm_attnproj<<<dim3(DM/128, NTOK/128), 256, 0, stream>>>(ctxb, Wapb, b_aproj, hidden, hs);
-    ln_kernel<<<NTOK, 256, 0, stream>>>(hs, ln2_g, ln2_b, x, xb);
-    router_kernel<<<NTOK, 64, 0, stream>>>(x, w_rout, cnt, expTok, tokE, tokPos, tokGate);
+    ln_b<<<NTOK, 256, 0, stream>>>(hidden, ln1_g, ln1_b, xb);
+    mm_qkv<<<dim3(TDIM/128, NTOK/64), 256, 0, stream>>>(xb, Wab, b_attn, Qb, Kb, Vt);
+    fattn<<<NB*NHEAD*32, 64, 0, stream>>>(Qb, Kb, Vt, ctxb);
+    mm_attnproj<<<dim3(DM/64, NTOK/64), 256, 0, stream>>>(ctxb, Wapb, b_aproj, hidden, hs);
+    ln_router<<<NTOK, 256, 0, stream>>>(hs, ln2_g, ln2_b, w_rout, xb,
+                                        cnt, expTok, tokE, tokPos, tokGate);
     offsets_kernel<<<1, 64, 0, stream>>>(cnt, offE);
     mm_fc<<<dim3(FF/128, NTOK/128, NEXP), 256, 0, stream>>>(xb, Wfcb, b_fc, expTok, cnt, offE, H);
-    mm_proj<<<dim3(DM/128, NTOK/128, NEXP), 256, 0, stream>>>(H, Wprb, cnt, offE, Y);
-    combine_kernel<<<NTOK, 256, 0, stream>>>(hs, Y, b_proj, tokE, tokPos, tokGate, offE, out);
-}
+    mm_proj<<<dim3((DM/128)*2, NTOK/64, NEXP), 256, 0, stream>>>(H, Wprb, cnt, offE, Yp);
+    combine_kernel<<<NTOK, 256, 0, stream>>>(hs, Yp, b_proj, tokE, tokPos, tokGate, offE, out);
+}
```

Measured after the change: 481.8 us. 1.08x faster.
